# Kernel optimization log

Hardware: AMD Instinct MI355X
Metric: run time of the kernel (lower is better)

Reference implementation:

```python
import jax, jax.numpy as jnp
import numpy as np

B, T, D, E, L, MAXP, PRED, TOPK = 128, 2048, 256, 32, 8, 168, 168, 2
INIT_STD = 0.02


def setup_inputs() -> dict:
    key = jax.random.key(0)
    ks = jax.random.split(key, 18)
    n = jax.random.normal
    s = INIT_STD
    inp = {
        "ctx_embed": n(ks[0], (B, T, D), jnp.float32),
        "query_experts": n(ks[1], (E, MAXP, D), jnp.float32) * s,
        "query_pos": n(ks[2], (MAXP, D), jnp.float32) * s,
        "len_emb": n(ks[3], (MAXP + 1, D), jnp.float32),  # nn.Embedding table
        "latents": n(ks[4], (L, D), jnp.float32) * s,
        "w_lat_q": n(ks[5], (D, D), jnp.float32) / np.sqrt(D),
        "w_ctx_k": n(ks[6], (D, D), jnp.float32) / np.sqrt(D),
        "w_ctx_v": n(ks[7], (D, D), jnp.float32) / np.sqrt(D),
        "w_lat_out": n(ks[8], (D, D), jnp.float32) / np.sqrt(D),
        "w_step_q": n(ks[9], (D, D), jnp.float32) / np.sqrt(D),
        "w_lat_k": n(ks[10], (D, D), jnp.float32) / np.sqrt(D),
        "w_lat_v": n(ks[11], (D, D), jnp.float32) / np.sqrt(D),
        "w_step_out": n(ks[12], (D, D), jnp.float32) / np.sqrt(D),
        "gate_w1": n(ks[13], (2 * D, D), jnp.float32) / np.sqrt(2 * D),
        "gate_b1": jnp.zeros((D,), jnp.float32),
        "gate_w2": n(ks[14], (D, E), jnp.float32) / np.sqrt(D),
        "gate_b2": jnp.zeros((E,), jnp.float32),
        "pred_len": PRED,
    }
    return inp


def _sdpa_1head(q, k, v):
    # q: [B,Q,D], k/v: [B,K,D]; single-head scaled dot-product attention
    scale = jnp.asarray(q.shape[-1], q.dtype) ** -0.5
    attn = jax.nn.softmax(jnp.einsum('bqd,bkd->bqk', q, k) * scale, axis=-1)
    return jnp.einsum('bqk,bkd->bqd', attn, v)


def reference(ctx_embed, query_experts, query_pos, len_emb, latents,
              w_lat_q, w_ctx_k, w_ctx_v, w_lat_out,
              w_step_q, w_lat_k, w_lat_v, w_step_out,
              gate_w1, gate_b1, gate_w2, gate_b2, pred_len):
    Bb, Tt, Dd = ctx_embed.shape
    P = pred_len

    # step base: positional queries + pred-length embedding
    pos = query_pos[:P][None]                      # [1,P,D]
    len_vec = len_emb[P][None, None]               # [1,1,D]
    step_base = jnp.broadcast_to(pos + len_vec, (Bb, P, Dd))

    # latent <- context cross-attention
    lat = jnp.broadcast_to(latents[None], (Bb, latents.shape[0], Dd))
    q1 = lat @ w_lat_q
    k1 = ctx_embed @ w_ctx_k
    v1 = ctx_embed @ w_ctx_v
    lat_ctx = _sdpa_1head(q1, k1, v1) @ w_lat_out  # [B,L,D]

    # step <- latent cross-attention
    q2 = step_base @ w_step_q
    k2 = lat_ctx @ w_lat_k
    v2 = lat_ctx @ w_lat_v
    step_ctx = _sdpa_1head(q2, k2, v2) @ w_step_out  # [B,P,D]

    # gating MLP over [step_base, step_ctx]
    gate_inp = jnp.concatenate([step_base, step_ctx], axis=-1)  # [B,P,2D]
    h = jax.nn.gelu(gate_inp @ gate_w1 + gate_b1, approximate=False)
    logits = h @ gate_w2 + gate_b2                               # [B,P,E]

    # top-k masking + softmax (keep top-k logits, others -> -inf)
    topv = jax.lax.top_k(logits, TOPK)[0]
    kth = topv[..., -1:]
    masked = jnp.where(logits >= kth, logits, -jnp.inf)
    weights = jax.nn.softmax(masked, axis=-1)                    # [B,P,E]

    # mixture of expert queries (einsum avoids [B,P,E,D] intermediate)
    queries = jnp.einsum('bpe,epd->bpd', weights, query_experts[:, :P, :])
    return queries
```

## Files before the change

kernel.cpp:

```cpp
#include <hip/hip_runtime.h>
#include <math.h>

#define NB 128
#define NT 2048
#define ND 256
#define NE 32
#define NL 8
#define NP 168
#define SCL 0.0625f

#define OFF_QK   0
#define OFF_LATQ 2048
#define OFF_WVO  4096
#define OFF_WSO1 69632
#define OFF_WVW  135168
#define OFF_G0   200704
#define OFF_Q2S  243712
#define OFF_AV   286720
#define OFF_DEN  2383872
#define OFF_K2   2392064
#define OFF_VW   2654208

typedef __attribute__((ext_vector_type(8))) short short8b;
typedef __attribute__((ext_vector_type(4))) float f32x4;

static __device__ __forceinline__ unsigned short f2bf(float f){
  unsigned u = __float_as_uint(f);
  u += 0x7fffu + ((u >> 16) & 1u);
  return (unsigned short)(u >> 16);
}

static __device__ __forceinline__ short8b pack8(float4 lo, float4 hi){
  short8b r;
  r[0]=(short)f2bf(lo.x); r[1]=(short)f2bf(lo.y); r[2]=(short)f2bf(lo.z); r[3]=(short)f2bf(lo.w);
  r[4]=(short)f2bf(hi.x); r[5]=(short)f2bf(hi.y); r[6]=(short)f2bf(hi.z); r[7]=(short)f2bf(hi.w);
  return r;
}

__global__ __launch_bounds__(256) void pre1(const float* __restrict__ latents,
    const float* __restrict__ wlq, const float* __restrict__ wcv,
    const float* __restrict__ wlo, const float* __restrict__ wso,
    const float* __restrict__ gw1, const float* __restrict__ gb1,
    const float* __restrict__ qpos, const float* __restrict__ lemb,
    const float* __restrict__ wsq, float* __restrict__ ws)
{
  int bid = blockIdx.x, tid = threadIdx.x;
  if (bid < 256){
    const float* a = wcv + bid*ND;
    float acc = 0.f;
    #pragma unroll 8
    for (int k=0;k<ND;k++) acc += a[k]*wlo[k*ND+tid];
    ws[OFF_WVO + bid*ND + tid] = acc;
  } else if (bid < 512){
    int i = bid-256;
    const float* a = wso + i*ND;
    float acc = 0.f;
    #pragma unroll 8
    for (int k=0;k<ND;k++) acc += a[k]*gw1[(ND+k)*ND+tid];
    ws[OFF_WSO1 + i*ND + tid] = acc;
  } else if (bid < 512+NP){
    int p = bid-512;
    float ag = gb1[tid], aq = 0.f;
    #pragma unroll 4
    for (int j=0;j<ND;j++){
      float sb = qpos[p*ND+j] + lemb[NP*ND+j];
      ag += sb*gw1[j*ND+tid];
      aq += sb*wsq[j*ND+tid];
    }
    ws[OFF_G0  + p*ND + tid] = ag;
    ws[OFF_Q2S + p*ND + tid] = aq*SCL;
  } else {
    int l = bid-(512+NP);
    float acc = 0.f;
    #pragma unroll 8
    for (int m=0;m<ND;m++) acc += latents[l*ND+m]*wlq[m*ND+tid];
    ws[OFF_LATQ + l*ND + tid] = acc;
  }
}

__global__ __launch_bounds__(256) void pre2(const float* __restrict__ wck,
                                            const float* __restrict__ wlv,
                                            float* __restrict__ ws)
{
  int bid = blockIdx.x, tid = threadIdx.x;
  if (bid < 256){
    int d = bid;
    float wk = wck[d*ND + tid];
    float part[NL];
    #pragma unroll
    for (int l=0;l<NL;l++) part[l] = ws[OFF_LATQ + l*ND + tid]*wk;
    #pragma unroll
    for (int m=1;m<64;m<<=1){
      #pragma unroll
      for (int l=0;l<NL;l++) part[l] += __shfl_xor(part[l], m);
    }
    __shared__ float red[4][NL];
    if ((tid&63)==0){
      #pragma unroll
      for (int l=0;l<NL;l++) red[tid>>6][l] = part[l];
    }
    __syncthreads();
    if (tid < NL){
      float s = red[0][tid]+red[1][tid]+red[2][tid]+red[3][tid];
      ws[OFF_QK + tid*ND + d] = s*SCL;
    }
  } else {
    int dd = bid - 256;
    const float* a = wlv + dd*ND;
    float acc = 0.f;
    #pragma unroll 8
    for (int k=0;k<ND;k++) acc += a[k]*ws[OFF_WSO1 + k*ND + tid];
    ws[OFF_WVW + dd*ND + tid] = acc;
  }
}

__global__ __launch_bounds__(256) void kA(const float* __restrict__ ctx, float* __restrict__ ws)
{
  __shared__ float ctile[64*256];
  __shared__ float efull[256*8];

  int bid = blockIdx.x;
  int b = bid >> 3, sp = bid & 7;
  int tid = threadIdx.x;
  int wv = tid >> 6, lane = tid & 63;
  int c = lane & 15, g = lane >> 4;
  int dq = lane;

  short8b afrag[8];
  if (c < NL){
    const float* qk = ws + OFF_QK + c*ND + g*8;
    #pragma unroll
    for (int kk=0;kk<8;kk++){
      float4 lo = *(const float4*)(qk + kk*32);
      float4 hi = *(const float4*)(qk + kk*32 + 4);
      afrag[kk] = pack8(lo, hi);
    }
  } else {
    short8b z;
    #pragma unroll
    for (int j=0;j<8;j++) z[j] = 0;
    #pragma unroll
    for (int kk=0;kk<8;kk++) afrag[kk] = z;
  }

  float av[8][4];
  #pragma unroll
  for (int l=0;l<8;l++){
    #pragma unroll
    for (int j=0;j<4;j++) av[l][j] = 0.f;
  }

  const int T0 = sp*256;
  #pragma unroll 1
  for (int sub=0; sub<4; ++sub){
    int rr = wv*16 + c;
    int r7 = rr & 7;
    const float* cp = ctx + ((size_t)(b*NT + T0 + sub*64 + rr))*ND + g*8;
    float4 lo[8], hi[8];
    #pragma unroll
    for (int kk=0;kk<8;kk++){
      lo[kk] = *(const float4*)(cp + kk*32);
      hi[kk] = *(const float4*)(cp + kk*32 + 4);
    }
    float* crow = ctile + rr*256;
    #pragma unroll
    for (int kk=0;kk<8;kk++){
      int slo = 2*g + 8*kk;
      *(float4*)(crow + (((slo  ) ^ r7)<<2)) = lo[kk];
      *(float4*)(crow + (((slo+1) ^ r7)<<2)) = hi[kk];
    }
    f32x4 acc = {0.f,0.f,0.f,0.f};
    #pragma unroll
    for (int kk=0;kk<8;kk++)
      acc = __builtin_amdgcn_mfma_f32_16x16x32_bf16(afrag[kk], pack8(lo[kk],hi[kk]), acc, 0, 0, 0);
    if (g < 2){
      float4 ev = make_float4(__expf(acc[0]),__expf(acc[1]),__expf(acc[2]),__expf(acc[3]));
      *(float4*)&efull[(sub*64 + rr)*8 + g*4] = ev;
    }
    __syncthreads();
    #pragma unroll
    for (int i=0;i<16;i++){
      int tl = wv*16 + i;
      float4 c4 = *(const float4*)(ctile + tl*256 + ((dq ^ (tl&7))<<2));
      const float* ep = efull + (sub*64 + tl)*8;
      float4 e0 = *(const float4*)ep;
      float4 e1 = *(const float4*)(ep+4);
      float e8[8];
      e8[0]=e0.x; e8[1]=e0.y; e8[2]=e0.z; e8[3]=e0.w;
      e8[4]=e1.x; e8[5]=e1.y; e8[6]=e1.z; e8[7]=e1.w;
      #pragma unroll
      for (int l=0;l<8;l++){
        av[l][0] += e8[l]*c4.x;
        av[l][1] += e8[l]*c4.y;
        av[l][2] += e8[l]*c4.z;
        av[l][3] += e8[l]*c4.w;
      }
    }
    __syncthreads();
  }

  float* red = ctile;
  #pragma unroll
  for (int l=0;l<8;l++)
    *(float4*)(red + (((l*4 + wv)*64 + dq)<<2)) = make_float4(av[l][0],av[l][1],av[l][2],av[l][3]);

  if (wv == 0){
    float dpart[8];
    #pragma unroll
    for (int l=0;l<8;l++) dpart[l] = 0.f;
    #pragma unroll
    for (int q=0;q<4;q++){
      const float* ep = efull + (q*64 + lane)*8;
      float4 e0 = *(const float4*)ep;
      float4 e1 = *(const float4*)(ep+4);
      dpart[0]+=e0.x; dpart[1]+=e0.y; dpart[2]+=e0.z; dpart[3]+=e0.w;
      dpart[4]+=e1.x; dpart[5]+=e1.y; dpart[6]+=e1.z; dpart[7]+=e1.w;
    }
    #pragma unroll
    for (int m=1;m<64;m<<=1){
      #pragma unroll
      for (int l=0;l<8;l++) dpart[l] += __shfl_xor(dpart[l], m);
    }
    if (lane == 0){
      #pragma unroll
      for (int l=0;l<8;l++) ws[OFF_DEN + bid*8 + l] = dpart[l];
    }
  }
  __syncthreads();

  #pragma unroll
  for (int rep=0; rep<2; ++rep){
    int lidx = tid + rep*256;
    int l = lidx >> 6, d2 = lidx & 63;
    float4 s0 = *(const float4*)(red + (((l*4 + 0)*64 + d2)<<2));
    float4 s1 = *(const float4*)(red + (((l*4 + 1)*64 + d2)<<2));
    float4 s2 = *(const float4*)(red + (((l*4 + 2)*64 + d2)<<2));
    float4 s3 = *(const float4*)(red + (((l*4 + 3)*64 + d2)<<2));
    float4 o;
    o.x = s0.x+s1.x+s2.x+s3.x;
    o.y = s0.y+s1.y+s2.y+s3.y;
    o.z = s0.z+s1.z+s2.z+s3.z;
    o.w = s0.w+s1.w+s2.w+s3.w;
    *(float4*)&ws[OFF_AV + ((size_t)(bid*8 + l))*ND + d2*4] = o;
  }
}

__global__ __launch_bounds__(256) void kB1(const float* __restrict__ wlk,
                                           float* __restrict__ ws)
{
  int bid = blockIdx.x;
  int b = bid >> 1, half = bid & 1;
  int d = threadIdx.x;
  __shared__ float avnT[256][8];
  __shared__ float latT[256][8];

  float dent[8];
  #pragma unroll
  for (int l=0;l<8;l++){
    float s = 0.f;
    #pragma unroll
    for (int sp=0;sp<8;sp++) s += ws[OFF_DEN + (b*8+sp)*8 + l];
    dent[l] = s;
  }
  float av8[8];
  #pragma unroll
  for (int l=0;l<8;l++){
    float s = 0.f;
    #pragma unroll
    for (int sp=0;sp<8;sp++) s += ws[OFF_AV + ((size_t)((b*8+sp)*8 + l))*ND + d];
    av8[l] = s / dent[l];
  }
  *(float4*)&avnT[d][0] = make_float4(av8[0],av8[1],av8[2],av8[3]);
  *(float4*)&avnT[d][4] = make_float4(av8[4],av8[5],av8[6],av8[7]);
  __syncthreads();

  float lc[8];
  #pragma unroll
  for (int l=0;l<8;l++) lc[l] = 0.f;
  #pragma unroll 8
  for (int dd=0;dd<ND;dd++){
    float w = ws[OFF_WVO + dd*ND + d];
    float4 a0 = *(const float4*)&avnT[dd][0];
    float4 a1 = *(const float4*)&avnT[dd][4];
    lc[0]+=a0.x*w; lc[1]+=a0.y*w; lc[2]+=a0.z*w; lc[3]+=a0.w*w;
    lc[4]+=a1.x*w; lc[5]+=a1.y*w; lc[6]+=a1.z*w; lc[7]+=a1.w*w;
  }
  *(float4*)&latT[d][0] = make_float4(lc[0],lc[1],lc[2],lc[3]);
  *(float4*)&latT[d][4] = make_float4(lc[4],lc[5],lc[6],lc[7]);
  __syncthreads();

  const float* w3 = half ? (ws + OFF_WVW) : wlk;
  float o8[8];
  #pragma unroll
  for (int l=0;l<8;l++) o8[l] = 0.f;
  #pragma unroll 8
  for (int dd=0;dd<ND;dd++){
    float w = w3[dd*ND + d];
    float4 a0 = *(const float4*)&latT[dd][0];
    float4 a1 = *(const float4*)&latT[dd][4];
    o8[0]+=a0.x*w; o8[1]+=a0.y*w; o8[2]+=a0.z*w; o8[3]+=a0.w*w;
    o8[4]+=a1.x*w; o8[5]+=a1.y*w; o8[6]+=a1.z*w; o8[7]+=a1.w*w;
  }
  size_t obase = (half ? OFF_VW : OFF_K2) + (size_t)b*8*ND + d;
  #pragma unroll
  for (int l=0;l<8;l++) ws[obase + l*ND] = o8[l];
}

__global__ __launch_bounds__(256) void kB2(const float* __restrict__ ws,
    const float* __restrict__ gw2, const float* __restrict__ gb2,
    const float* __restrict__ qe, float* __restrict__ out)
{
  int bid = blockIdx.x;
  int b = bid / 6, p0 = (bid % 6)*28;
  int tid = threadIdx.x;

  __shared__ float q2h[28][260];
  __shared__ float k2s[8][260];
  __shared__ float vws[8][260];
  __shared__ float wexp[28][8];
  __shared__ float lg[28][33];
  __shared__ float4 sel[28];

  #pragma unroll
  for (int i=0;i<7;i++){
    int idx = tid + i*256;
    int r = idx >> 6, c4 = idx & 63;
    *(float4*)&q2h[r][c4*4] = *(const float4*)&ws[OFF_Q2S + (p0+r)*ND + c4*4];
  }
  #pragma unroll
  for (int i=0;i<2;i++){
    int idx = tid + i*256;
    int l = idx >> 6, c4 = idx & 63;
    *(float4*)&k2s[l][c4*4] = *(const float4*)&ws[OFF_K2 + (b*8+l)*ND + c4*4];
    *(float4*)&vws[l][c4*4] = *(const float4*)&ws[OFF_VW + (b*8+l)*ND + c4*4];
  }
  __syncthreads();

  {
    int pp = tid >> 3, l1 = tid & 7;
    if (pp < 28){
      float s2 = 0.f;
      #pragma unroll 8
      for (int i=0;i<64;i++){
        float4 qa = *(const float4*)&q2h[pp][4*i];
        float4 kb = *(const float4*)&k2s[l1][4*i];
        s2 += qa.x*kb.x + qa.y*kb.y + qa.z*kb.z + qa.w*kb.w;
      }
      float e2 = __expf(s2);
      float den = e2;
      den += __shfl_xor(den,1); den += __shfl_xor(den,2); den += __shfl_xor(den,4);
      wexp[pp][l1] = e2/den;
    }
  }
  __syncthreads();

  {
    float vcol[8];
    #pragma unroll
    for (int l=0;l<8;l++) vcol[l] = vws[l][tid];
    #pragma unroll 4
    for (int p=0;p<28;p++){
      float4 w0 = *(const float4*)&wexp[p][0];
      float4 w1v = *(const float4*)&wexp[p][4];
      float x = ws[OFF_G0 + (p0+p)*ND + tid]
              + w0.x*vcol[0]+w0.y*vcol[1]+w0.z*vcol[2]+w0.w*vcol[3]
              + w1v.x*vcol[4]+w1v.y*vcol[5]+w1v.z*vcol[6]+w1v.w*vcol[7];
      q2h[p][tid] = 0.5f*x*(1.f+erff(x*0.70710678118654752f));
    }
  }
  __syncthreads();

  {
    int e = tid & 31, pq = tid >> 5;
    if (pq < 7){
      float b2v = gb2[e];
      float a0=b2v, a1=b2v, a2=b2v, a3=b2v;
      for (int cc=0;cc<ND;cc+=4){
        float w20 = gw2[(cc+0)*NE + e];
        float w21 = gw2[(cc+1)*NE + e];
        float w22 = gw2[(cc+2)*NE + e];
        float w23 = gw2[(cc+3)*NE + e];
        float4 h0 = *(const float4*)&q2h[pq*4+0][cc];
        float4 h1 = *(const float4*)&q2h[pq*4+1][cc];
        float4 h2 = *(const float4*)&q2h[pq*4+2][cc];
        float4 h3 = *(const float4*)&q2h[pq*4+3][cc];
        a0 += h0.x*w20 + h0.y*w21 + h0.z*w22 + h0.w*w23;
        a1 += h1.x*w20 + h1.y*w21 + h1.z*w22 + h1.w*w23;
        a2 += h2.x*w20 + h2.y*w21 + h2.z*w22 + h2.w*w23;
        a3 += h3.x*w20 + h3.y*w21 + h3.z*w22 + h3.w*w23;
      }
      lg[pq*4+0][e] = a0;
      lg[pq*4+1][e] = a1;
      lg[pq*4+2][e] = a2;
      lg[pq*4+3][e] = a3;
    }
  }
  __syncthreads();

  if (tid < 28){
    float m1 = -1e30f, m2 = -1e30f;
    int e1 = 0, ee2 = 0;
    for (int e3=0;e3<NE;e3++){
      float v = lg[tid][e3];
      if (v > m1){ m2 = m1; ee2 = e1; m1 = v; e1 = e3; }
      else if (v > m2){ m2 = v; ee2 = e3; }
    }
    float z = __expf(m2 - m1);
    float inv = 1.f/(1.f+z);
    sel[tid] = make_float4(__int_as_float(e1), __int_as_float(ee2), inv, z*inv);
  }
  __syncthreads();

  for (int p=0;p<28;p++){
    float4 s = sel[p];
    int e1 = __float_as_int(s.x), ee2 = __float_as_int(s.y);
    float q1v = qe[((size_t)e1*NP + (p0+p))*ND + tid];
    float q2v = qe[((size_t)ee2*NP + (p0+p))*ND + tid];
    out[((size_t)b*NP + (p0+p))*ND + tid] = s.z*q1v + s.w*q2v;
  }
}

extern "C" void kernel_launch(void* const* d_in, const int* in_sizes, int n_in,
                              void* d_out, int out_size, void* d_ws, size_t ws_size,
                              hipStream_t stream)
{
  const float* ctx  = (const float*)d_in[0];
  const float* qe   = (const float*)d_in[1];
  const float* qpos = (const float*)d_in[2];
  const float* lemb = (const float*)d_in[3];
  const float* lat  = (const float*)d_in[4];
  const float* wlq  = (const float*)d_in[5];
  const float* wck  = (const float*)d_in[6];
  const float* wcv  = (const float*)d_in[7];
  const float* wlo  = (const float*)d_in[8];
  const float* wsq  = (const float*)d_in[9];
  const float* wlk  = (const float*)d_in[10];
  const float* wlv  = (const float*)d_in[11];
  const float* wso  = (const float*)d_in[12];
  const float* gw1  = (const float*)d_in[13];
  const float* gb1  = (const float*)d_in[14];
  const float* gw2  = (const float*)d_in[15];
  const float* gb2  = (const float*)d_in[16];
  float* out = (float*)d_out;
  float* ws  = (float*)d_ws;

  pre1<<<512+NP+NL, 256, 0, stream>>>(lat, wlq, wcv, wlo, wso, gw1, gb1, qpos, lemb, wsq, ws);
  pre2<<<512, 256, 0, stream>>>(wck, wlv, ws);
  kA  <<<NB*8, 256, 0, stream>>>(ctx, ws);
  kB1 <<<NB*2, 256, 0, stream>>>(wlk, ws);
  kB2 <<<NB*6, 256, 0, stream>>>(ws, gw2, gb2, qe, out);
}
```

Baseline: 154.0 us.

## Warp-specialize kA into producer/consumer waves with double-buffered context tiles

The main context-attention kernel changes from 1024 blocks of 256 threads to 256 blocks of 512 threads. Four producer waves load 64-row context tiles into a double-buffered LDS and compute the exp scores with MFMA, while four consumer waves accumulate the weighted values from the other buffer. Each block now covers half a sequence, so there are fewer partial sums for kB1 to reduce and a smaller workspace. The cost is fewer blocks in flight and one LDS-heavy block per CU, which may limit memory-latency hiding on a kernel dominated by loading the 256MB context.

```diff
diff --git a/kernel.cpp b/kernel.cpp
--- a/kernel.cpp
+++ b/kernel.cpp
@@ -17,9 +17,9 @@
 #define OFF_G0   200704
 #define OFF_Q2S  243712
 #define OFF_AV   286720
-#define OFF_DEN  2383872
-#define OFF_K2   2392064
-#define OFF_VW   2654208
+#define OFF_DEN  811008
+#define OFF_K2   813056
+#define OFF_VW   1075200
 
 typedef __attribute__((ext_vector_type(8))) short short8b;
 typedef __attribute__((ext_vector_type(4))) float f32x4;
@@ -114,124 +114,127 @@
   }
 }
 
-__global__ __launch_bounds__(256) void kA(const float* __restrict__ ctx, float* __restrict__ ws)
-{
-  __shared__ float ctile[64*256];
-  __shared__ float efull[256*8];
+__global__ __launch_bounds__(512,1) void kA(const float* __restrict__ ctx, float* __restrict__ ws)
+{
+  __shared__ float buf[2][64*256];
+  __shared__ float ebuf[2][64][8];
+  __shared__ float denred[4][8];
 
   int bid = blockIdx.x;
-  int b = bid >> 3, sp = bid & 7;
+  int b = bid >> 1, half = bid & 1;
   int tid = threadIdx.x;
-  int wv = tid >> 6, lane = tid & 63;
-  int c = lane & 15, g = lane >> 4;
-  int dq = lane;
+  int wid = tid >> 6, lane = tid & 63;
+  const size_t rowbase = (size_t)(b*NT + half*1024);
+
+  int pr = wid;
+  int c = lane & 15, g = lane >> 4, c7 = c & 7;
+  int cw = wid - 4, dq = lane;
 
   short8b afrag[8];
-  if (c < NL){
-    const float* qk = ws + OFF_QK + c*ND + g*8;
-    #pragma unroll
-    for (int kk=0;kk<8;kk++){
-      float4 lo = *(const float4*)(qk + kk*32);
-      float4 hi = *(const float4*)(qk + kk*32 + 4);
-      afrag[kk] = pack8(lo, hi);
-    }
-  } else {
-    short8b z;
-    #pragma unroll
-    for (int j=0;j<8;j++) z[j] = 0;
-    #pragma unroll
-    for (int kk=0;kk<8;kk++) afrag[kk] = z;
+  if (wid < 4){
+    if (c < NL){
+      const float* qk = ws + OFF_QK + c*ND + g*8;
+      #pragma unroll
+      for (int kk=0;kk<8;kk++){
+        float4 lo = *(const float4*)(qk + kk*32);
+        float4 hi = *(const float4*)(qk + kk*32 + 4);
+        afrag[kk] = pack8(lo, hi);
+      }
+    } else {
+      short8b z;
+      #pragma unroll
+      for (int j=0;j<8;j++) z[j] = 0;
+      #pragma unroll
+      for (int kk=0;kk<8;kk++) afrag[kk] = z;
+    }
   }
 
   float av[8][4];
+  float den8[8];
   #pragma unroll
   for (int l=0;l<8;l++){
+    den8[l] = 0.f;
     #pragma unroll
     for (int j=0;j<4;j++) av[l][j] = 0.f;
   }
 
-  const int T0 = sp*256;
+#define PRODUCE(TB, SOFF) do{                                                      \
+    const float* rs_ = ctx + (rowbase + (size_t)(SOFF)*64 + pr*16)*ND;             \
+    float* myrows_ = &buf[TB][pr*16*256];                                          \
+    float4 st_[8];                                                                 \
+    _Pragma("unroll")                                                              \
+    for (int i_=0;i_<8;i_++) st_[i_] = *(const float4*)(rs_ + (size_t)i_*ND + lane*4); \
+    _Pragma("unroll")                                                              \
+    for (int i_=0;i_<8;i_++) *(float4*)(myrows_ + i_*256 + ((lane ^ i_)<<2)) = st_[i_]; \
+    _Pragma("unroll")                                                              \
+    for (int i_=0;i_<8;i_++) st_[i_] = *(const float4*)(rs_ + (size_t)(i_+8)*ND + lane*4); \
+    _Pragma("unroll")                                                              \
+    for (int i_=0;i_<8;i_++) *(float4*)(myrows_ + (i_+8)*256 + ((lane ^ i_)<<2)) = st_[i_]; \
+    f32x4 acc_ = {0.f,0.f,0.f,0.f};                                                \
+    const float* brow_ = &buf[TB][(pr*16 + c)*256];                                \
+    _Pragma("unroll")                                                              \
+    for (int kk_=0;kk_<8;kk_++){                                                   \
+      int sA_ = 2*g + 8*kk_;                                                       \
+      float4 lo_ = *(const float4*)(brow_ + (((sA_  ) ^ c7)<<2));                  \
+      float4 hi_ = *(const float4*)(brow_ + (((sA_+1) ^ c7)<<2));                  \
+      acc_ = __builtin_amdgcn_mfma_f32_16x16x32_bf16(afrag[kk_], pack8(lo_,hi_), acc_, 0, 0, 0); \
+    }                                                                              \
+    if (g < 2){                                                                    \
+      float4 ev_ = make_float4(__expf(acc_[0]),__expf(acc_[1]),__expf(acc_[2]),__expf(acc_[3])); \
+      *(float4*)&ebuf[TB][pr*16 + c][g*4] = ev_;                                   \
+    }                                                                              \
+  }while(0)
+
+#define CONSUME(CB) do{                                                            \
+    _Pragma("unroll")                                                              \
+    for (int i_=0;i_<16;i_++){                                                     \
+      int tl_ = cw*16 + i_;                                                        \
+      float4 c4_ = *(const float4*)(&buf[CB][tl_*256] + ((dq ^ (tl_&7))<<2));      \
+      const float* ep_ = &ebuf[CB][tl_][0];                                        \
+      float4 e0_ = *(const float4*)ep_;                                            \
+      float4 e1_ = *(const float4*)(ep_+4);                                        \
+      av[0][0]+=e0_.x*c4_.x; av[0][1]+=e0_.x*c4_.y; av[0][2]+=e0_.x*c4_.z; av[0][3]+=e0_.x*c4_.w; \
+      av[1][0]+=e0_.y*c4_.x; av[1][1]+=e0_.y*c4_.y; av[1][2]+=e0_.y*c4_.z; av[1][3]+=e0_.y*c4_.w; \
+      av[2][0]+=e0_.z*c4_.x; av[2][1]+=e0_.z*c4_.y; av[2][2]+=e0_.z*c4_.z; av[2][3]+=e0_.z*c4_.w; \
+      av[3][0]+=e0_.w*c4_.x; av[3][1]+=e0_.w*c4_.y; av[3][2]+=e0_.w*c4_.z; av[3][3]+=e0_.w*c4_.w; \
+      av[4][0]+=e1_.x*c4_.x; av[4][1]+=e1_.x*c4_.y; av[4][2]+=e1_.x*c4_.z; av[4][3]+=e1_.x*c4_.w; \
+      av[5][0]+=e1_.y*c4_.x; av[5][1]+=e1_.y*c4_.y; av[5][2]+=e1_.y*c4_.z; av[5][3]+=e1_.y*c4_.w; \
+      av[6][0]+=e1_.z*c4_.x; av[6][1]+=e1_.z*c4_.y; av[6][2]+=e1_.z*c4_.z; av[6][3]+=e1_.z*c4_.w; \
+      av[7][0]+=e1_.w*c4_.x; av[7][1]+=e1_.w*c4_.y; av[7][2]+=e1_.w*c4_.z; av[7][3]+=e1_.w*c4_.w; \
+      den8[0]+=e0_.x; den8[1]+=e0_.y; den8[2]+=e0_.z; den8[3]+=e0_.w;              \
+      den8[4]+=e1_.x; den8[5]+=e1_.y; den8[6]+=e1_.z; den8[7]+=e1_.w;              \
+    }                                                                              \
+  }while(0)
+
+  if (wid < 4) PRODUCE(0, 0);
+  __syncthreads();
+
   #pragma unroll 1
-  for (int sub=0; sub<4; ++sub){
-    int rr = wv*16 + c;
-    int r7 = rr & 7;
-    const float* cp = ctx + ((size_t)(b*NT + T0 + sub*64 + rr))*ND + g*8;
-    float4 lo[8], hi[8];
+  for (int s=0; s<16; ++s){
+    if (wid < 4){
+      if (s < 15) PRODUCE((s+1)&1, s+1);
+    } else {
+      CONSUME(s&1);
+    }
+    __syncthreads();
+  }
+#undef PRODUCE
+#undef CONSUME
+
+  float* red = &buf[0][0];
+  if (wid >= 4){
     #pragma unroll
-    for (int kk=0;kk<8;kk++){
-      lo[kk] = *(const float4*)(cp + kk*32);
-      hi[kk] = *(const float4*)(cp + kk*32 + 4);
-    }
-    float* crow = ctile + rr*256;
-    #pragma unroll
-    for (int kk=0;kk<8;kk++){
-      int slo = 2*g + 8*kk;
-      *(float4*)(crow + (((slo  ) ^ r7)<<2)) = lo[kk];
-      *(float4*)(crow + (((slo+1) ^ r7)<<2)) = hi[kk];
-    }
-    f32x4 acc = {0.f,0.f,0.f,0.f};
-    #pragma unroll
-    for (int kk=0;kk<8;kk++)
-      acc = __builtin_amdgcn_mfma_f32_16x16x32_bf16(afrag[kk], pack8(lo[kk],hi[kk]), acc, 0, 0, 0);
-    if (g < 2){
-      float4 ev = make_float4(__expf(acc[0]),__expf(acc[1]),__expf(acc[2]),__expf(acc[3]));
-      *(float4*)&efull[(sub*64 + rr)*8 + g*4] = ev;
-    }
-    __syncthreads();
-    #pragma unroll
-    for (int i=0;i<16;i++){
-      int tl = wv*16 + i;
-      float4 c4 = *(const float4*)(ctile + tl*256 + ((dq ^ (tl&7))<<2));
-      const float* ep = efull + (sub*64 + tl)*8;
-      float4 e0 = *(const float4*)ep;
-      float4 e1 = *(const float4*)(ep+4);
-      float e8[8];
-      e8[0]=e0.x; e8[1]=e0.y; e8[2]=e0.z; e8[3]=e0.w;
-      e8[4]=e1.x; e8[5]=e1.y; e8[6]=e1.z; e8[7]=e1.w;
-      #pragma unroll
-      for (int l=0;l<8;l++){
-        av[l][0] += e8[l]*c4.x;
-        av[l][1] += e8[l]*c4.y;
-        av[l][2] += e8[l]*c4.z;
-        av[l][3] += e8[l]*c4.w;
-      }
-    }
-    __syncthreads();
-  }
-
-  float* red = ctile;
-  #pragma unroll
-  for (int l=0;l<8;l++)
-    *(float4*)(red + (((l*4 + wv)*64 + dq)<<2)) = make_float4(av[l][0],av[l][1],av[l][2],av[l][3]);
-
-  if (wv == 0){
-    float dpart[8];
-    #pragma unroll
-    for (int l=0;l<8;l++) dpart[l] = 0.f;
-    #pragma unroll
-    for (int q=0;q<4;q++){
-      const float* ep = efull + (q*64 + lane)*8;
-      float4 e0 = *(const float4*)ep;
-      float4 e1 = *(const float4*)(ep+4);
-      dpart[0]+=e0.x; dpart[1]+=e0.y; dpart[2]+=e0.z; dpart[3]+=e0.w;
-      dpart[4]+=e1.x; dpart[5]+=e1.y; dpart[6]+=e1.z; dpart[7]+=e1.w;
-    }
-    #pragma unroll
-    for (int m=1;m<64;m<<=1){
-      #pragma unroll
-      for (int l=0;l<8;l++) dpart[l] += __shfl_xor(dpart[l], m);
-    }
+    for (int l=0;l<8;l++)
+      *(float4*)(red + (((l*4 + cw)*64 + dq)<<2)) = make_float4(av[l][0],av[l][1],av[l][2],av[l][3]);
     if (lane == 0){
       #pragma unroll
-      for (int l=0;l<8;l++) ws[OFF_DEN + bid*8 + l] = dpart[l];
-    }
-  }
-  __syncthreads();
-
-  #pragma unroll
-  for (int rep=0; rep<2; ++rep){
-    int lidx = tid + rep*256;
-    int l = lidx >> 6, d2 = lidx & 63;
+      for (int l=0;l<8;l++) denred[cw][l] = den8[l];
+    }
+  }
+  __syncthreads();
+
+  {
+    int l = tid >> 6, d2 = tid & 63;
     float4 s0 = *(const float4*)(red + (((l*4 + 0)*64 + d2)<<2));
     float4 s1 = *(const float4*)(red + (((l*4 + 1)*64 + d2)<<2));
     float4 s2 = *(const float4*)(red + (((l*4 + 2)*64 + d2)<<2));
@@ -243,13 +246,15 @@
     o.w = s0.w+s1.w+s2.w+s3.w;
     *(float4*)&ws[OFF_AV + ((size_t)(bid*8 + l))*ND + d2*4] = o;
   }
+  if (tid < NL)
+    ws[OFF_DEN + bid*8 + tid] = denred[0][tid]+denred[1][tid]+denred[2][tid]+denred[3][tid];
 }
 
 __global__ __launch_bounds__(256) void kB1(const float* __restrict__ wlk,
                                            float* __restrict__ ws)
 {
   int bid = blockIdx.x;
-  int b = bid >> 1, half = bid & 1;
+  int b = bid >> 1, role = bid & 1;
   int d = threadIdx.x;
   __shared__ float avnT[256][8];
   __shared__ float latT[256][8];
@@ -257,18 +262,14 @@
   float dent[8];
   #pragma unroll
   for (int l=0;l<8;l++){
-    float s = 0.f;
-    #pragma unroll
-    for (int sp=0;sp<8;sp++) s += ws[OFF_DEN + (b*8+sp)*8 + l];
-    dent[l] = s;
+    dent[l] = ws[OFF_DEN + (b*2+0)*8 + l] + ws[OFF_DEN + (b*2+1)*8 + l];
   }
   float av8[8];
   #pragma unroll
   for (int l=0;l<8;l++){
-    float s = 0.f;
-    #pragma unroll
-    for (int sp=0;sp<8;sp++) s += ws[OFF_AV + ((size_t)((b*8+sp)*8 + l))*ND + d];
-    av8[l] = s / dent[l];
+    av8[l] = ws[OFF_AV + ((size_t)((b*2+0)*8 + l))*ND + d]
+           + ws[OFF_AV + ((size_t)((b*2+1)*8 + l))*ND + d];
+    av8[l] /= dent[l];
   }
   *(float4*)&avnT[d][0] = make_float4(av8[0],av8[1],av8[2],av8[3]);
   *(float4*)&avnT[d][4] = make_float4(av8[4],av8[5],av8[6],av8[7]);
@@ -289,7 +290,7 @@
   *(float4*)&latT[d][4] = make_float4(lc[4],lc[5],lc[6],lc[7]);
   __syncthreads();
 
-  const float* w3 = half ? (ws + OFF_WVW) : wlk;
+  const float* w3 = role ? (ws + OFF_WVW) : wlk;
   float o8[8];
   #pragma unroll
   for (int l=0;l<8;l++) o8[l] = 0.f;
@@ -301,7 +302,7 @@
     o8[0]+=a0.x*w; o8[1]+=a0.y*w; o8[2]+=a0.z*w; o8[3]+=a0.w*w;
     o8[4]+=a1.x*w; o8[5]+=a1.y*w; o8[6]+=a1.z*w; o8[7]+=a1.w*w;
   }
-  size_t obase = (half ? OFF_VW : OFF_K2) + (size_t)b*8*ND + d;
+  size_t obase = (role ? OFF_VW : OFF_K2) + (size_t)b*8*ND + d;
   #pragma unroll
   for (int l=0;l<8;l++) ws[obase + l*ND] = o8[l];
 }
@@ -331,8 +332,8 @@
   for (int i=0;i<2;i++){
     int idx = tid + i*256;
     int l = idx >> 6, c4 = idx & 63;
-    *(float4*)&k2s[l][c4*4] = *(const float4*)&ws[OFF_K2 + (b*8+l)*ND + c4*4];
-    *(float4*)&vws[l][c4*4] = *(const float4*)&ws[OFF_VW + (b*8+l)*ND + c4*4];
+    *(float4*)&k2s[l][c4*4] = *(const float4*)&ws[OFF_K2 + (size_t)(b*8+l)*ND + c4*4];
+    *(float4*)&vws[l][c4*4] = *(const float4*)&ws[OFF_VW + (size_t)(b*8+l)*ND + c4*4];
   }
   __syncthreads();
 
@@ -446,7 +447,7 @@
 
   pre1<<<512+NP+NL, 256, 0, stream>>>(lat, wlq, wcv, wlo, wso, gw1, gb1, qpos, lemb, wsq, ws);
   pre2<<<512, 256, 0, stream>>>(wck, wlv, ws);
-  kA  <<<NB*8, 256, 0, stream>>>(ctx, ws);
+  kA  <<<256, 512, 0, stream>>>(ctx, ws);
   kB1 <<<NB*2, 256, 0, stream>>>(wlk, ws);
   kB2 <<<NB*6, 256, 0, stream>>>(ws, gw2, gb2, qe, out);
 }
```

After: 202.2 us. 1.31x slower.
